# Optimization experiments

Hardware: AMD Instinct MI355X
Metric: run time of the kernel (lower is better)

## Reference

```python
import jax, jax.numpy as jnp
import numpy as np

N_NODES = 50000

def gcn_conv(x, W, b, row, col, ew, n):
    # PyG GCNConv: linear first (no bias in lin), then gcn_norm with added
    # self-loops (weight 1.0), symmetric D^{-1/2} normalization, scatter-add
    # aggregation from row (source) to col (target), then bias.
    h = x @ W                                      # [N, out]
    loop = jnp.arange(n, dtype=row.dtype)
    row_f = jnp.concatenate([row, loop])
    col_f = jnp.concatenate([col, loop])
    ew_f = jnp.concatenate([ew, jnp.ones((n,), dtype=ew.dtype)])
    deg = jax.ops.segment_sum(ew_f, col_f, num_segments=n)
    dinv = jnp.where(deg > 0, jax.lax.rsqrt(jnp.maximum(deg, 1e-30)), 0.0)
    norm = dinv[row_f] * ew_f * dinv[col_f]        # [E+N]
    msg = norm[:, None] * h[row_f]                 # gather + scale
    out = jax.ops.segment_sum(msg, col_f, num_segments=n)  # scatter-add
    return out + b

def setup_inputs() -> dict:
    key = jax.random.key(0)
    k = jax.random.split(key, 8)
    in_dim, hidden_dim, out_dim = 128, 256, 128
    n, e = N_NODES, 600000
    x = jax.random.normal(k[0], (n, in_dim), dtype=jnp.float32)
    edge_index = jax.random.randint(k[1], (2, e), 0, n, dtype=jnp.int64)
    edge_weight = jax.random.uniform(k[2], (e,), dtype=jnp.float32)
    # Glorot-style params (PyG GCNConv lin has no bias; bias added after aggregation)
    W1 = jax.random.normal(k[3], (in_dim, hidden_dim), dtype=jnp.float32) / np.sqrt(in_dim)
    b1 = jnp.zeros((hidden_dim,), dtype=jnp.float32)
    W2 = jax.random.normal(k[4], (hidden_dim, out_dim), dtype=jnp.float32) / np.sqrt(hidden_dim)
    b2 = jnp.zeros((out_dim,), dtype=jnp.float32)
    return {"x": x, "edge_index": edge_index, "edge_weight": edge_weight,
            "W1": W1, "b1": b1, "W2": W2, "b2": b2}

def reference(x, edge_index, edge_weight, W1, b1, W2, b2):
    n = x.shape[0]
    row, col = edge_index[0], edge_index[1]
    h = jax.nn.relu(gcn_conv(x, W1, b1, row, col, edge_weight, n))
    # dropout is identity in eval mode
    out = jax.nn.relu(gcn_conv(h, W2, b2, row, col, edge_weight, n))
    return out
```

## Files before the change

### kernel.cpp

```cpp
#include <hip/hip_runtime.h>
#include <hip/hip_bf16.h>

constexpr int IN_DIM  = 128;
constexpr int HID     = 256;
constexpr int OUT_DIM = 128;
constexpr int ELL_W   = 64;

typedef __attribute__((ext_vector_type(8))) short short8;
typedef __attribute__((ext_vector_type(8))) unsigned short ushort8;
typedef __attribute__((ext_vector_type(4))) float f32x4;

__device__ __forceinline__ float bf2f(unsigned short u) {
    return __uint_as_float(((unsigned int)u) << 16);
}
__device__ __forceinline__ unsigned short f2bf(float f) {
    unsigned int u = __float_as_uint(f);
    u += 0x7FFFu + ((u >> 16) & 1u);
    return (unsigned short)(u >> 16);
}
__device__ __forceinline__ unsigned short f2h(float f) {
    _Float16 h = (_Float16)f;
    unsigned short b;
    __builtin_memcpy(&b, &h, 2);
    return b;
}
__device__ __forceinline__ float h2f(unsigned short b) {
    _Float16 h;
    __builtin_memcpy(&h, &b, 2);
    return (float)h;
}
__device__ __forceinline__ unsigned int pack_e(int src, float w) {
    return (unsigned int)src | ((unsigned int)f2h(w) << 16);
}

__global__ void k_prep(int* __restrict__ cnt, int n,
                       const float* __restrict__ W1, unsigned short* __restrict__ w1t,
                       const float* __restrict__ W2, unsigned short* __restrict__ w2t) {
    const int i = blockIdx.x * 256 + threadIdx.x;
    if (i < n) cnt[i] = 0;
    if (i < IN_DIM * HID) {
        const int k = i / HID, nn = i % HID;
        w1t[(size_t)nn * IN_DIM + k] = f2bf(W1[i]);
    }
    if (i < HID * OUT_DIM) {
        const int k = i / OUT_DIM, nn = i % OUT_DIM;
        w2t[(size_t)nn * HID + k] = f2bf(W2[i]);
    }
}

__global__ void k_fill_ell(const int* __restrict__ row, const int* __restrict__ col,
                           const float* __restrict__ ew, int* __restrict__ cnt,
                           unsigned int* __restrict__ ell, int E) {
    const int i  = blockIdx.x * blockDim.x + threadIdx.x;
    const int e0 = i * 4;
    if (e0 + 3 < E) {
        const int4   c4 = *reinterpret_cast<const int4*>(col + e0);
        const int4   r4 = *reinterpret_cast<const int4*>(row + e0);
        const float4 w4 = *reinterpret_cast<const float4*>(ew + e0);
        const int p0 = atomicAdd(&cnt[c4.x], 1);
        const int p1 = atomicAdd(&cnt[c4.y], 1);
        const int p2 = atomicAdd(&cnt[c4.z], 1);
        const int p3 = atomicAdd(&cnt[c4.w], 1);
        if (p0 < ELL_W) ell[(size_t)c4.x * ELL_W + p0] = pack_e(r4.x, w4.x);
        if (p1 < ELL_W) ell[(size_t)c4.y * ELL_W + p1] = pack_e(r4.y, w4.y);
        if (p2 < ELL_W) ell[(size_t)c4.z * ELL_W + p2] = pack_e(r4.z, w4.z);
        if (p3 < ELL_W) ell[(size_t)c4.w * ELL_W + p3] = pack_e(r4.w, w4.w);
    } else {
        for (int e = e0; e < E; ++e) {
            const int c = col[e];
            const int p = atomicAdd(&cnt[c], 1);
            if (p < ELL_W) ell[(size_t)c * ELL_W + p] = pack_e(row[e], ew[e]);
        }
    }
}

__global__ __launch_bounds__(256)
void k_deg_xs(const int* __restrict__ cnt, const unsigned int* __restrict__ ell,
              const float* __restrict__ x, float* __restrict__ dinv,
              unsigned short* __restrict__ xs, int n) {
    const int wave = threadIdx.x >> 6;
    const int lane = threadIdx.x & 63;
    const int node = blockIdx.x * 4 + wave;
    if (node >= n) return;
    const int m = min(cnt[node], ELL_W);
    float s = (lane < m) ? h2f((unsigned short)(ell[(size_t)node * ELL_W + lane] >> 16)) : 0.f;
    #pragma unroll
    for (int d = 32; d; d >>= 1) s += __shfl_xor(s, d);
    const float di = rsqrtf(1.0f + s);
    if (lane == 0) dinv[node] = di;
    const float2 v = *reinterpret_cast<const float2*>(x + (size_t)node * IN_DIM + lane * 2);
    const unsigned int packed = (unsigned int)f2bf(v.x * di) |
                                ((unsigned int)f2bf(v.y * di) << 16);
    *reinterpret_cast<unsigned int*>(xs + (size_t)node * IN_DIM + lane * 2) = packed;
}

template<bool BIAS_RELU, bool BF16OUT>
__global__ __launch_bounds__(256)
void k_gather_w(const int* __restrict__ cnt, const unsigned int* __restrict__ ell,
                const float* __restrict__ dinv, const unsigned short* __restrict__ hs,
                const float* __restrict__ bias, void* __restrict__ out_, int n) {
    constexpr int F = 128;
    const int wave  = threadIdx.x >> 6;
    const int lane  = threadIdx.x & 63;
    const int group = lane >> 4;
    const int j8    = (lane & 15) * 8;
    const int node  = blockIdx.x * 4 + wave;
    if (node >= n) return;

    const int m = min(cnt[node], ELL_W);
    const unsigned int* bucket = ell + (size_t)node * ELL_W;

    float acc[8] = {};
    int p = group;
    for (; p + 4 < m; p += 8) {
        const unsigned int m0 = bucket[p], m1 = bucket[p + 4];
        const ushort8 v0 = *reinterpret_cast<const ushort8*>(hs + (size_t)(m0 & 0xFFFFu) * F + j8);
        const ushort8 v1 = *reinterpret_cast<const ushort8*>(hs + (size_t)(m1 & 0xFFFFu) * F + j8);
        const float w0 = h2f((unsigned short)(m0 >> 16));
        const float w1 = h2f((unsigned short)(m1 >> 16));
        #pragma unroll
        for (int i = 0; i < 8; ++i) acc[i] = fmaf(w0, bf2f(v0[i]), acc[i]);
        #pragma unroll
        for (int i = 0; i < 8; ++i) acc[i] = fmaf(w1, bf2f(v1[i]), acc[i]);
    }
    if (p < m) {
        const unsigned int m0 = bucket[p];
        const ushort8 v0 = *reinterpret_cast<const ushort8*>(hs + (size_t)(m0 & 0xFFFFu) * F + j8);
        const float w0 = h2f((unsigned short)(m0 >> 16));
        #pragma unroll
        for (int i = 0; i < 8; ++i) acc[i] = fmaf(w0, bf2f(v0[i]), acc[i]);
    }

    #pragma unroll
    for (int i = 0; i < 8; ++i) {
        acc[i] += __shfl_xor(acc[i], 16);
        acc[i] += __shfl_xor(acc[i], 32);
    }

    if (group == 0) {
        const float dc = dinv[node];
        const ushort8 hv = *reinterpret_cast<const ushort8*>(hs + (size_t)node * F + j8);
        float o[8];
        if (BIAS_RELU) {
            const float4 b0 = *reinterpret_cast<const float4*>(bias + j8);
            const float4 b1 = *reinterpret_cast<const float4*>(bias + j8 + 4);
            const float bb[8] = {b0.x, b0.y, b0.z, b0.w, b1.x, b1.y, b1.z, b1.w};
            #pragma unroll
            for (int i = 0; i < 8; ++i)
                o[i] = fmaxf(fmaf(dc, acc[i] + bf2f(hv[i]), bb[i]), 0.f);
        } else {
            #pragma unroll
            for (int i = 0; i < 8; ++i) o[i] = dc * (acc[i] + bf2f(hv[i]));
        }
        if (BF16OUT) {
            ushort ob[8];
            #pragma unroll
            for (int i = 0; i < 8; ++i) ob[i] = f2bf(o[i]);
            *reinterpret_cast<uint4*>((unsigned short*)out_ + (size_t)node * F + j8) =
                *reinterpret_cast<uint4*>(ob);
        } else {
            float* op = (float*)out_ + (size_t)node * F + j8;
            *reinterpret_cast<float4*>(op)     = make_float4(o[0], o[1], o[2], o[3]);
            *reinterpret_cast<float4*>(op + 4) = make_float4(o[4], o[5], o[6], o[7]);
        }
    }
}

template<bool BIAS_RELU, bool ROWSCALE>
__global__ __launch_bounds__(256)
void k_mfma_gemm(const unsigned short* __restrict__ A,
                 const unsigned short* __restrict__ Bt,
                 const float* __restrict__ bias, const float* __restrict__ dinv,
                 unsigned short* __restrict__ C, int M, int N, int K) {
    __shared__ ushort As[128 * 64];
    __shared__ ushort Bs[128 * 64];

    const int t    = threadIdx.x;
    const int w    = t >> 6;
    const int lane = t & 63;
    const int quad = lane >> 4;
    const int l16  = lane & 15;
    const int wm   = w >> 1;
    const int wn   = w & 1;
    const int rowBase = blockIdx.y * 128;
    const int colBase = blockIdx.x * 128;

    const ushort* gA = A  + (size_t)(rowBase + w * 32 + lane / 8) * K + (lane % 8) * 8;
    const ushort* gB = Bt + (size_t)(colBase + w * 32 + lane / 8) * K + (lane % 8) * 8;
    ushort* lA = &As[(w * 32) * 64];
    ushort* lB = &Bs[(w * 32) * 64];

    f32x4 acc[4][4] = {};

    for (int k0 = 0; k0 < K; k0 += 64) {
        #pragma unroll
        for (int j = 0; j < 4; ++j) {
            __builtin_amdgcn_global_load_lds(
                (const __attribute__((address_space(1))) uint32_t*)(gA + k0 + (size_t)j * 8 * K),
                (__attribute__((address_space(3))) uint32_t*)(lA + j * 8 * 64), 16, 0, 0);
            __builtin_amdgcn_global_load_lds(
                (const __attribute__((address_space(1))) uint32_t*)(gB + k0 + (size_t)j * 8 * K),
                (__attribute__((address_space(3))) uint32_t*)(lB + j * 8 * 64), 16, 0, 0);
        }
        __syncthreads();

        #pragma unroll
        for (int ks = 0; ks < 2; ++ks) {
            short8 af[4], bf[4];
            #pragma unroll
            for (int mt = 0; mt < 4; ++mt)
                af[mt] = *(const short8*)&As[(wm * 64 + mt * 16 + l16) * 64 + ks * 32 + quad * 8];
            #pragma unroll
            for (int nt = 0; nt < 4; ++nt)
                bf[nt] = *(const short8*)&Bs[(wn * 64 + nt * 16 + l16) * 64 + ks * 32 + quad * 8];
            #pragma unroll
            for (int mt = 0; mt < 4; ++mt)
                #pragma unroll
                for (int nt = 0; nt < 4; ++nt)
                    acc[mt][nt] = __builtin_amdgcn_mfma_f32_16x16x32_bf16(
                        af[mt], bf[nt], acc[mt][nt], 0, 0, 0);
        }
        __syncthreads();
    }

    float bv[4];
    if (BIAS_RELU) {
        #pragma unroll
        for (int nt = 0; nt < 4; ++nt)
            bv[nt] = bias[colBase + wn * 64 + nt * 16 + l16];
    }
    #pragma unroll
    for (int mt = 0; mt < 4; ++mt) {
        #pragma unroll
        for (int i = 0; i < 4; ++i) {
            const int r = rowBase + wm * 64 + mt * 16 + quad * 4 + i;
            if (r < M) {
                const float dr = ROWSCALE ? dinv[r] : 1.0f;
                #pragma unroll
                for (int nt = 0; nt < 4; ++nt) {
                    const int c = colBase + wn * 64 + nt * 16 + l16;
                    float v = acc[mt][nt][i];
                    if (BIAS_RELU) v = fmaxf(v + bv[nt], 0.f);
                    if (ROWSCALE)  v *= dr;
                    C[(size_t)r * N + c] = f2bf(v);
                }
            }
        }
    }
}

extern "C" void kernel_launch(void* const* d_in, const int* in_sizes, int n_in,
                              void* d_out, int out_size, void* d_ws, size_t ws_size,
                              hipStream_t stream) {
    const float* x  = (const float*)d_in[0];
    const int*   ei = (const int*)d_in[1];
    const float* ew = (const float*)d_in[2];
    const float* W1 = (const float*)d_in[3];
    const float* b1 = (const float*)d_in[4];
    const float* W2 = (const float*)d_in[5];
    const float* b2 = (const float*)d_in[6];
    float* out = (float*)d_out;

    const int n = in_sizes[0] / IN_DIM;
    const int E = in_sizes[1] / 2;
    const int Mpad = (n + 127) & ~127;
    const int* row = ei;
    const int* col = ei + E;

    float* ws = (float*)d_ws;
    size_t o = 0;
    auto alloc = [&](size_t words) { float* p = ws + o; o += (words + 63) & ~(size_t)63; return p; };
    float* dinv = alloc(n);
    int*   cnt  = (int*)alloc(n);
    unsigned int* ell = (unsigned int*)alloc((size_t)n * ELL_W);
    unsigned short* xs   = (unsigned short*)alloc((size_t)Mpad * IN_DIM / 2);
    unsigned short* aggx = (unsigned short*)alloc((size_t)Mpad * IN_DIM / 2);
    unsigned short* h1   = (unsigned short*)alloc((size_t)Mpad * HID / 2);
    unsigned short* h2s  = (unsigned short*)alloc((size_t)Mpad * OUT_DIM / 2);
    unsigned short* w1t  = (unsigned short*)alloc((size_t)IN_DIM * HID / 2);
    unsigned short* w2t  = (unsigned short*)alloc((size_t)HID * OUT_DIM / 2);

    k_prep<<<(n + 255) / 256, 256, 0, stream>>>(cnt, n, W1, w1t, W2, w2t);
    k_fill_ell<<<(E / 4 + 255) / 256, 256, 0, stream>>>(row, col, ew, cnt, ell, E);
    k_deg_xs<<<(n + 3) / 4, 256, 0, stream>>>(cnt, ell, x, dinv, xs, n);

    k_gather_w<false, true><<<(n + 3) / 4, 256, 0, stream>>>(cnt, ell, dinv, xs, nullptr, aggx, n);
    {
        dim3 grid(HID / 128, Mpad / 128);
        k_mfma_gemm<true, false><<<grid, 256, 0, stream>>>(aggx, w1t, b1, nullptr, h1, n, HID, IN_DIM);
    }

    {
        dim3 grid(OUT_DIM / 128, Mpad / 128);
        k_mfma_gemm<false, true><<<grid, 256, 0, stream>>>(h1, w2t, nullptr, dinv, h2s, n, OUT_DIM, HID);
    }
    k_gather_w<true, false><<<(n + 3) / 4, 256, 0, stream>>>(cnt, ell, dinv, h2s, b2, out, n);
}
```

Measured before the change: 215.6 us.

## Fuse the two dense GEMMs into one kernel keeping hidden activations in LDS

Replaces the two separate MFMA GEMM launches with a single kernel per 64-row tile. It computes relu(A·W1+b1) into shared memory as bf16, then multiplies that tile by W2 and scales by dinv. This removes the round trip of the 50000x256 hidden matrix through global memory and one kernel launch. It also adds an XOR swizzle on LDS addressing to reduce bank conflicts. The fused kernel uses about 72 KB of LDS and smaller row tiles, which may lower occupancy.

```diff
diff --git a/kernel.cpp b/kernel.cpp
--- a/kernel.cpp
+++ b/kernel.cpp
@@ -166,42 +166,43 @@
     }
 }
 
-template<bool BIAS_RELU, bool ROWSCALE>
 __global__ __launch_bounds__(256)
-void k_mfma_gemm(const unsigned short* __restrict__ A,
-                 const unsigned short* __restrict__ Bt,
-                 const float* __restrict__ bias, const float* __restrict__ dinv,
-                 unsigned short* __restrict__ C, int M, int N, int K) {
-    __shared__ ushort As[128 * 64];
-    __shared__ ushort Bs[128 * 64];
+void k_fused_gemm(const unsigned short* __restrict__ A,
+                  const unsigned short* __restrict__ W1t,
+                  const unsigned short* __restrict__ W2t,
+                  const float* __restrict__ b1,
+                  const float* __restrict__ dinv,
+                  unsigned short* __restrict__ H2,
+                  int M) {
+    __shared__ ushort As[64 * 64];
+    __shared__ ushort Bs[256 * 64];
+    __shared__ ushort Hs[64 * 256];
 
     const int t    = threadIdx.x;
     const int w    = t >> 6;
     const int lane = t & 63;
     const int quad = lane >> 4;
     const int l16  = lane & 15;
-    const int wm   = w >> 1;
-    const int wn   = w & 1;
-    const int rowBase = blockIdx.y * 128;
-    const int colBase = blockIdx.x * 128;
-
-    const ushort* gA = A  + (size_t)(rowBase + w * 32 + lane / 8) * K + (lane % 8) * 8;
-    const ushort* gB = Bt + (size_t)(colBase + w * 32 + lane / 8) * K + (lane % 8) * 8;
-    ushort* lA = &As[(w * 32) * 64];
-    ushort* lB = &Bs[(w * 32) * 64];
+    const int lrow = lane >> 3;
+    const int lcol = ((lane & 7) ^ lrow) * 8;
+    const int xr   = (l16 & 7) << 3;
+    const int rowBase = blockIdx.x * 64;
+
+    const ushort* gA  = A   + (size_t)(rowBase + w * 16 + lrow) * IN_DIM + lcol;
+    const ushort* gB1 = W1t + (size_t)(w * 64 + lrow) * IN_DIM + lcol;
 
     f32x4 acc[4][4] = {};
-
-    for (int k0 = 0; k0 < K; k0 += 64) {
-        #pragma unroll
-        for (int j = 0; j < 4; ++j) {
+    for (int k0 = 0; k0 < IN_DIM; k0 += 64) {
+        #pragma unroll
+        for (int j = 0; j < 2; ++j)
             __builtin_amdgcn_global_load_lds(
-                (const __attribute__((address_space(1))) uint32_t*)(gA + k0 + (size_t)j * 8 * K),
-                (__attribute__((address_space(3))) uint32_t*)(lA + j * 8 * 64), 16, 0, 0);
+                (const __attribute__((address_space(1))) uint32_t*)(gA + k0 + (size_t)j * 8 * IN_DIM),
+                (__attribute__((address_space(3))) uint32_t*)(&As[(w * 16 + j * 8) * 64]), 16, 0, 0);
+        #pragma unroll
+        for (int j = 0; j < 8; ++j)
             __builtin_amdgcn_global_load_lds(
-                (const __attribute__((address_space(1))) uint32_t*)(gB + k0 + (size_t)j * 8 * K),
-                (__attribute__((address_space(3))) uint32_t*)(lB + j * 8 * 64), 16, 0, 0);
-        }
+                (const __attribute__((address_space(1))) uint32_t*)(gB1 + k0 + (size_t)j * 8 * IN_DIM),
+                (__attribute__((address_space(3))) uint32_t*)(&Bs[(w * 64 + j * 8) * 64]), 16, 0, 0);
         __syncthreads();
 
         #pragma unroll
@@ -209,10 +210,10 @@
             short8 af[4], bf[4];
             #pragma unroll
             for (int mt = 0; mt < 4; ++mt)
-                af[mt] = *(const short8*)&As[(wm * 64 + mt * 16 + l16) * 64 + ks * 32 + quad * 8];
+                af[mt] = *(const short8*)&As[(mt * 16 + l16) * 64 + ((ks * 32 + quad * 8) ^ xr)];
             #pragma unroll
             for (int nt = 0; nt < 4; ++nt)
-                bf[nt] = *(const short8*)&Bs[(wn * 64 + nt * 16 + l16) * 64 + ks * 32 + quad * 8];
+                bf[nt] = *(const short8*)&Bs[(w * 64 + nt * 16 + l16) * 64 + ((ks * 32 + quad * 8) ^ xr)];
             #pragma unroll
             for (int mt = 0; mt < 4; ++mt)
                 #pragma unroll
@@ -223,30 +224,68 @@
         __syncthreads();
     }
 
-    float bv[4];
-    if (BIAS_RELU) {
-        #pragma unroll
-        for (int nt = 0; nt < 4; ++nt)
-            bv[nt] = bias[colBase + wn * 64 + nt * 16 + l16];
-    }
-    #pragma unroll
-    for (int mt = 0; mt < 4; ++mt) {
-        #pragma unroll
-        for (int i = 0; i < 4; ++i) {
-            const int r = rowBase + wm * 64 + mt * 16 + quad * 4 + i;
-            if (r < M) {
-                const float dr = ROWSCALE ? dinv[r] : 1.0f;
+    {
+        float bv[4];
+        #pragma unroll
+        for (int nt = 0; nt < 4; ++nt) bv[nt] = b1[w * 64 + nt * 16 + l16];
+        #pragma unroll
+        for (int mt = 0; mt < 4; ++mt)
+            #pragma unroll
+            for (int i = 0; i < 4; ++i) {
+                const int row = mt * 16 + quad * 4 + i;
+                const int xw  = (row & 7) << 3;
                 #pragma unroll
                 for (int nt = 0; nt < 4; ++nt) {
-                    const int c = colBase + wn * 64 + nt * 16 + l16;
-                    float v = acc[mt][nt][i];
-                    if (BIAS_RELU) v = fmaxf(v + bv[nt], 0.f);
-                    if (ROWSCALE)  v *= dr;
-                    C[(size_t)r * N + c] = f2bf(v);
+                    const int col = w * 64 + nt * 16 + l16;
+                    Hs[row * 256 + (col ^ xw)] = f2bf(fmaxf(acc[mt][nt][i] + bv[nt], 0.f));
                 }
             }
-        }
-    }
+    }
+    __syncthreads();
+
+    const ushort* gB2 = W2t + (size_t)(w * 32 + lrow) * HID + lcol;
+    f32x4 acc2[4][2] = {};
+    for (int k0 = 0; k0 < HID; k0 += 64) {
+        #pragma unroll
+        for (int j = 0; j < 4; ++j)
+            __builtin_amdgcn_global_load_lds(
+                (const __attribute__((address_space(1))) uint32_t*)(gB2 + k0 + (size_t)j * 8 * HID),
+                (__attribute__((address_space(3))) uint32_t*)(&Bs[(w * 32 + j * 8) * 64]), 16, 0, 0);
+        __syncthreads();
+
+        #pragma unroll
+        for (int ks = 0; ks < 2; ++ks) {
+            short8 af[4], bf[2];
+            #pragma unroll
+            for (int mt = 0; mt < 4; ++mt)
+                af[mt] = *(const short8*)&Hs[(mt * 16 + l16) * 256 + ((k0 + ks * 32 + quad * 8) ^ xr)];
+            #pragma unroll
+            for (int nt = 0; nt < 2; ++nt)
+                bf[nt] = *(const short8*)&Bs[(w * 32 + nt * 16 + l16) * 64 + ((ks * 32 + quad * 8) ^ xr)];
+            #pragma unroll
+            for (int mt = 0; mt < 4; ++mt)
+                #pragma unroll
+                for (int nt = 0; nt < 2; ++nt)
+                    acc2[mt][nt] = __builtin_amdgcn_mfma_f32_16x16x32_bf16(
+                        af[mt], bf[nt], acc2[mt][nt], 0, 0, 0);
+        }
+        __syncthreads();
+    }
+
+    #pragma unroll
+    for (int mt = 0; mt < 4; ++mt)
+        #pragma unroll
+        for (int i = 0; i < 4; ++i) {
+            const int r = rowBase + mt * 16 + quad * 4 + i;
+            if (r < M) {
+                const float dr = dinv[r];
+                #pragma unroll
+                for (int nt = 0; nt < 2; ++nt) {
+                    const int c = w * 32 + nt * 16 + l16;
+                    H2[(size_t)r * OUT_DIM + c] = f2bf(acc2[mt][nt][i] * dr);
+                }
+            }
+        }
 }
 
 extern "C" void kernel_launch(void* const* d_in, const int* in_sizes, int n_in,
@@ -275,7 +314,6 @@
     unsigned int* ell = (unsigned int*)alloc((size_t)n * ELL_W);
     unsigned short* xs   = (unsigned short*)alloc((size_t)Mpad * IN_DIM / 2);
     unsigned short* aggx = (unsigned short*)alloc((size_t)Mpad * IN_DIM / 2);
-    unsigned short* h1   = (unsigned short*)alloc((size_t)Mpad * HID / 2);
     unsigned short* h2s  = (unsigned short*)alloc((size_t)Mpad * OUT_DIM / 2);
     unsigned short* w1t  = (unsigned short*)alloc((size_t)IN_DIM * HID / 2);
     unsigned short* w2t  = (unsigned short*)alloc((size_t)HID * OUT_DIM / 2);
@@ -285,14 +323,8 @@
     k_deg_xs<<<(n + 3) / 4, 256, 0, stream>>>(cnt, ell, x, dinv, xs, n);
 
     k_gather_w<false, true><<<(n + 3) / 4, 256, 0, stream>>>(cnt, ell, dinv, xs, nullptr, aggx, n);
-    {
-        dim3 grid(HID / 128, Mpad / 128);
-        k_mfma_gemm<true, false><<<grid, 256, 0, stream>>>(aggx, w1t, b1, nullptr, h1, n, HID, IN_DIM);
-    }
-
-    {
-        dim3 grid(OUT_DIM / 128, Mpad / 128);
-        k_mfma_gemm<false, true><<<grid, 256, 0, stream>>>(h1, w2t, nullptr, dinv, h2s, n, OUT_DIM, HID);
-    }
+
+    k_fused_gemm<<<Mpad / 64, 256, 0, stream>>>(aggx, w1t, w2t, b1, dinv, h2s, n);
+
     k_gather_w<true, false><<<(n + 3) / 4, 256, 0, stream>>>(cnt, ell, dinv, h2s, b2, out, n);
 }
```

Measured after the change: 205.7 us. 4.6% less time.
